# Performance work log

Hardware: AMD Instinct MI355X
Metric: run time of the kernel (lower is better)

## Reference

```python
import jax, jax.numpy as jnp
import numpy as np

N = 50000
E = 800000
IN_DIM = 128
HID = 32
OUT_DIM = 64
HEADS = 4
NEG_SLOPE = 0.2  # DGL GATConv default leaky_relu slope


def setup_inputs() -> dict:
    key = jax.random.key(0)
    ks = jax.random.split(key, 16)
    h = jax.random.normal(ks[0], (N, IN_DIM), dtype=jnp.float32)
    src = jax.random.randint(ks[1], (E,), 0, N, dtype=jnp.int32)
    dst = jax.random.randint(ks[2], (E,), 0, N, dtype=jnp.int32)
    s = 0.05
    # layer 1: in 128 -> heads*32 = 128
    W1 = jax.random.normal(ks[3], (IN_DIM, HEADS * HID), dtype=jnp.float32) * s
    al1 = jax.random.normal(ks[4], (HEADS, HID), dtype=jnp.float32) * s
    ar1 = jax.random.normal(ks[5], (HEADS, HID), dtype=jnp.float32) * s
    # layer 2: in 128 -> heads*32 = 128
    W2 = jax.random.normal(ks[6], (HEADS * HID, HEADS * HID), dtype=jnp.float32) * s
    al2 = jax.random.normal(ks[7], (HEADS, HID), dtype=jnp.float32) * s
    ar2 = jax.random.normal(ks[8], (HEADS, HID), dtype=jnp.float32) * s
    # last layer: in 128 -> heads*64 = 256 (needs residual projection)
    W3 = jax.random.normal(ks[9], (HEADS * HID, HEADS * OUT_DIM), dtype=jnp.float32) * s
    al3 = jax.random.normal(ks[10], (HEADS, OUT_DIM), dtype=jnp.float32) * s
    ar3 = jax.random.normal(ks[11], (HEADS, OUT_DIM), dtype=jnp.float32) * s
    resW3 = jax.random.normal(ks[12], (HEADS * HID, HEADS * OUT_DIM), dtype=jnp.float32) * s
    return {"h": h, "W1": W1, "al1": al1, "ar1": ar1, "W2": W2, "al2": al2,
            "ar2": ar2, "W3": W3, "al3": al3, "ar3": ar3, "resW3": resW3,
            "src": src, "dst": dst}


def gat_layer(h, src, dst, W, al, ar, heads, out_feats, res_W=None, act=None):
    n = h.shape[0]
    feat = (h @ W).reshape(n, heads, out_feats)          # [N,H,D]
    el = jnp.einsum('nhd,hd->nh', feat, al)               # [N,H]
    er = jnp.einsum('nhd,hd->nh', feat, ar)               # [N,H]
    e = jax.nn.leaky_relu(el[src] + er[dst], NEG_SLOPE)   # [E,H]
    m = jax.ops.segment_max(e, dst, num_segments=n)       # per-dst max, [N,H]
    ex = jnp.exp(e - m[dst])
    denom = jax.ops.segment_sum(ex, dst, num_segments=n)  # [N,H]
    alpha = ex / denom[dst]                               # edge softmax, [E,H]
    msg = feat[src] * alpha[:, :, None]                   # [E,H,D]
    rst = jax.ops.segment_sum(msg, dst, num_segments=n)   # [N,H,D]
    res = (h @ res_W) if res_W is not None else h
    rst = rst + res.reshape(n, heads, out_feats)
    if act is not None:
        rst = act(rst)
    return rst


def reference(h, W1, al1, ar1, W2, al2, ar2, W3, al3, ar3, resW3, src, dst):
    n = h.shape[0]
    x = gat_layer(h, src, dst, W1, al1, ar1, HEADS, HID, act=jax.nn.relu)
    x = x.reshape(n, -1)
    # feat_drop=0.3 on layer 2 omitted (eval/deterministic mode)
    x = gat_layer(x, src, dst, W2, al2, ar2, HEADS, HID, act=jax.nn.relu)
    x = x.reshape(n, -1)
    x = gat_layer(x, src, dst, W3, al3, ar3, HEADS, OUT_DIM, res_W=resW3)
    return x.mean(axis=1)  # mean over heads -> [N, OUT_DIM]
```

## Files before the change

### kernel.cpp

```cpp
#include <hip/hip_runtime.h>
#include <hip/hip_bf16.h>
#include <math.h>


#define NEG_SLOPE 0.2f

typedef __attribute__((ext_vector_type(8))) __bf16 bf16x8;
typedef __attribute__((ext_vector_type(4))) float f32x4;

__device__ __forceinline__ float leaky(float x) { return fmaxf(x, NEG_SLOPE * x); }
__device__ __forceinline__ ushort f2bf(float f) {
    unsigned u = __float_as_uint(f);
    return (ushort)((u + 0x7fffu + ((u >> 16) & 1u)) >> 16);
}
__device__ __forceinline__ float bf2f(ushort b) { return __uint_as_float(((unsigned)b) << 16); }
__device__ __forceinline__ float lo16f(unsigned v) { return __uint_as_float(v << 16); }
__device__ __forceinline__ float hi16f(unsigned v) { return __uint_as_float(v & 0xffff0000u); }


__global__ void hist_kernel(const int* __restrict__ dst, int* __restrict__ deg, int E) {
    int i = blockIdx.x * blockDim.x + threadIdx.x;
    if (i < E) atomicAdd(&deg[dst[i]], 1);
}

__global__ void block_scan_kernel(const int* __restrict__ deg, int* __restrict__ loc,
                                  int* __restrict__ bsum, int n) {
    __shared__ int sm[1024];
    const int tid = threadIdx.x;
    const int i = blockIdx.x * 1024 + tid;
    int v = (i < n) ? deg[i] : 0;
    sm[tid] = v;
    __syncthreads();
    for (int off = 1; off < 1024; off <<= 1) {
        int t = (tid >= off) ? sm[tid - off] : 0;
        __syncthreads();
        sm[tid] += t;
        __syncthreads();
    }
    if (i < n) loc[i] = sm[tid] - v;
    if (tid == 1023) bsum[blockIdx.x] = sm[1023];
}

__global__ void apply_scan_kernel(const int* __restrict__ loc, const int* __restrict__ bsum,
                                  int* __restrict__ row_ptr, int* __restrict__ cursor,
                                  int n, int nb) {
    __shared__ int pb[64];
    const int tid = threadIdx.x;
    if (tid < 64) {
        int v = (tid < nb) ? bsum[tid] : 0;
        int orig = v;
        for (int off = 1; off < 64; off <<= 1) {
            int t = __shfl_up(v, off);
            if (tid >= off) v += t;
        }
        pb[tid] = v - orig;
        if (tid == 63 && blockIdx.x == 0) row_ptr[n] = v;
    }
    __syncthreads();
    int i = blockIdx.x * blockDim.x + tid;
    if (i < n) {
        int v = loc[i] + pb[i >> 10];
        row_ptr[i] = v;
        cursor[i]  = v;
    }
}

__global__ void scatter_kernel(const int* __restrict__ src, const int* __restrict__ dst,
                               int* __restrict__ cursor, int* __restrict__ ssrc, int E) {
    int i = blockIdx.x * blockDim.x + threadIdx.x;
    if (i < E) {
        int s = src[i];
        int pos = atomicAdd(&cursor[dst[i]], 1);
        ssrc[pos] = s;
    }
}


__global__ void prep_kernel(const float* __restrict__ h, ushort* __restrict__ xbh,
                            const float* __restrict__ W1, ushort* __restrict__ W1th,
                            const float* __restrict__ W2, ushort* __restrict__ W2th,
                            const float* __restrict__ W3, ushort* __restrict__ W3th,
                            const float* __restrict__ rW3, ushort* __restrict__ rWmh,
                            int* __restrict__ cursor, int nh4, int n) {
    int i = blockIdx.x * blockDim.x + threadIdx.x;
    if (i < nh4) {
        float4 v = ((const float4*)h)[i];
        ushort4 o;
        o.x = f2bf(v.x); o.y = f2bf(v.y); o.z = f2bf(v.z); o.w = f2bf(v.w);
        ((ushort4*)xbh)[i] = o;
        return;
    }
    int j = i - nh4;
    if (j < 16384) {
        int c = j >> 7, k = j & 127;
        int kd = k ^ ((c & 7) << 3);
        W1th[c * 128 + kd] = f2bf(W1[k * 128 + c]);
    } else if (j < 32768) {
        j -= 16384;
        int c = j >> 7, k = j & 127;
        int kd = k ^ ((c & 7) << 3);
        W2th[c * 128 + kd] = f2bf(W2[k * 128 + c]);
    } else if (j < 65536) {
        j -= 32768;
        int c = j >> 7, k = j & 127;
        int kd = k ^ ((c & 7) << 3);
        W3th[c * 128 + kd] = f2bf(W3[k * 256 + c]);
    } else if (j < 73728) {
        j -= 65536;
        int c = j >> 7, k = j & 127;
        const float* row = rW3 + (size_t)k * 256;
        float v = 0.25f * ((row[c] + row[64 + c]) + (row[128 + c] + row[192 + c]));
        int kd = k ^ ((c & 7) << 3);
        rWmh[c * 128 + kd] = f2bf(v);
    } else if (j < 73728 + n) {
        cursor[j - 73728] = 0;
    }
}


__global__ void __launch_bounds__(128)
gemm_kernel(const ushort* __restrict__ Ah, const ushort* __restrict__ Bth,
            const ushort* __restrict__ B2th,
            ushort* __restrict__ Cb, float* __restrict__ C2f,
            const float* __restrict__ alv, const float* __restrict__ arv,
            float* __restrict__ el, float* __restrict__ er,
            int M, int Ncols, int dshift) {
    extern __shared__ ushort Ws[];
    ushort* Ws2 = Ws + 128 * 128;
    const int tid = threadIdx.x;
    const int wv = tid >> 6;
    const int lane = tid & 63;
    const int l15 = lane & 15;
    const int g = lane >> 4;
    const int bm = blockIdx.x * 64 + wv * 32;
    const int bn = blockIdx.y * 128;
    const bool do2 = (B2th != nullptr) && (blockIdx.y == 0);

    {
        const uint4* gh = (const uint4*)(Bth + (size_t)bn * 128);
        uint4* sh = (uint4*)Ws;
#pragma unroll
        for (int it = 0; it < 16; ++it) sh[it * 128 + tid] = gh[it * 128 + tid];
        if (do2) {
            const uint4* g2 = (const uint4*)B2th;
            uint4* s2 = (uint4*)Ws2;
#pragma unroll
            for (int it = 0; it < 8; ++it) s2[it * 128 + tid] = g2[it * 128 + tid];
        }
    }
    __syncthreads();

    const int m0 = bm + l15;
    const int m1 = bm + 16 + l15;
    const int mc0 = (m0 < M) ? m0 : (M - 1);
    const int mc1 = (m1 < M) ? m1 : (M - 1);
    bf16x8 xh[2][4];
#pragma unroll
    for (int kk = 0; kk < 4; ++kk) {
        xh[0][kk] = *(const bf16x8*)(Ah + (size_t)mc0 * 128 + kk * 32 + g * 8);
        xh[1][kk] = *(const bf16x8*)(Ah + (size_t)mc1 * 128 + kk * 32 + g * 8);
    }

    f32x4 acc[2][8] = {};
    f32x4 acc2[2][4] = {};
    const int swz = (l15 & 7) << 4;
#pragma unroll
    for (int n = 0; n < 8; ++n) {
        const int colb = (n * 16 + l15) * 256;
#pragma unroll
        for (int kk = 0; kk < 4; ++kk) {
            const int boff = colb + ((kk * 64 + g * 16) ^ swz);
            bf16x8 wh = *(const bf16x8*)((const char*)Ws + boff);
            acc[0][n] = __builtin_amdgcn_mfma_f32_16x16x32_bf16(wh, xh[0][kk], acc[0][n], 0, 0, 0);
            acc[1][n] = __builtin_amdgcn_mfma_f32_16x16x32_bf16(wh, xh[1][kk], acc[1][n], 0, 0, 0);
        }
    }
    if (do2) {
#pragma unroll
        for (int n = 0; n < 4; ++n) {
            const int colb = (n * 16 + l15) * 256;
#pragma unroll
            for (int kk = 0; kk < 4; ++kk) {
                const int boff = colb + ((kk * 64 + g * 16) ^ swz);
                bf16x8 w2 = *(const bf16x8*)((const char*)Ws2 + boff);
                acc2[0][n] = __builtin_amdgcn_mfma_f32_16x16x32_bf16(w2, xh[0][kk], acc2[0][n], 0, 0, 0);
                acc2[1][n] = __builtin_amdgcn_mfma_f32_16x16x32_bf16(w2, xh[1][kk], acc2[1][n], 0, 0, 0);
            }
        }
    }

#pragma unroll
    for (int mf = 0; mf < 2; ++mf) {
        const int m = (mf == 0) ? m0 : m1;
        const bool valid = (m < M);
        if (valid) {
            size_t ro = (size_t)m * Ncols;
#pragma unroll
            for (int n = 0; n < 8; ++n) {
                int col = bn + n * 16 + g * 4;
                ushort4 o;
                o.x = f2bf(acc[mf][n][0]); o.y = f2bf(acc[mf][n][1]);
                o.z = f2bf(acc[mf][n][2]); o.w = f2bf(acc[mf][n][3]);
                *(ushort4*)&Cb[ro + col] = o;
            }
            if (do2) {
#pragma unroll
                for (int n = 0; n < 4; ++n) {
                    *(float4*)&C2f[(size_t)m * 64 + n * 16 + g * 4] =
                        make_float4(acc2[mf][n][0], acc2[mf][n][1],
                                    acc2[mf][n][2], acc2[mf][n][3]);
                }
            }
        }
        if (alv) {
            float e0 = 0.f, e1 = 0.f, e2 = 0.f, e3 = 0.f;
            float r0 = 0.f, r1 = 0.f, r2 = 0.f, r3 = 0.f;
            const bool four = (dshift == 5);
#pragma unroll
            for (int n = 0; n < 8; ++n) {
                float se = 0.f, sr = 0.f;
#pragma unroll
                for (int rr = 0; rr < 4; ++rr) {
                    int col = bn + n * 16 + g * 4 + rr;
                    float c = acc[mf][n][rr];
                    se += c * alv[col];
                    sr += c * arv[col];
                }
                if (four) {
                    if (n < 2)      { e0 += se; r0 += sr; }
                    else if (n < 4) { e1 += se; r1 += sr; }
                    else if (n < 6) { e2 += se; r2 += sr; }
                    else            { e3 += se; r3 += sr; }
                } else {
                    if (n < 4)      { e0 += se; r0 += sr; }
                    else            { e1 += se; r1 += sr; }
                }
            }
            e0 += __shfl_xor(e0, 16); e0 += __shfl_xor(e0, 32);
            e1 += __shfl_xor(e1, 16); e1 += __shfl_xor(e1, 32);
            r0 += __shfl_xor(r0, 16); r0 += __shfl_xor(r0, 32);
            r1 += __shfl_xor(r1, 16); r1 += __shfl_xor(r1, 32);
            if (four) {
                e2 += __shfl_xor(e2, 16); e2 += __shfl_xor(e2, 32);
                e3 += __shfl_xor(e3, 16); e3 += __shfl_xor(e3, 32);
                r2 += __shfl_xor(r2, 16); r2 += __shfl_xor(r2, 32);
                r3 += __shfl_xor(r3, 16); r3 += __shfl_xor(r3, 32);
            }
            if (valid && g == 0) {
                if (four) {
                    el[m * 4 + 0] = e0; el[m * 4 + 1] = e1;
                    el[m * 4 + 2] = e2; el[m * 4 + 3] = e3;
                    er[m * 4 + 0] = r0; er[m * 4 + 1] = r1;
                    er[m * 4 + 2] = r2; er[m * 4 + 3] = r3;
                } else {
                    int h0 = bn >> 6;
                    el[m * 4 + h0] = e0; el[m * 4 + h0 + 1] = e1;
                    er[m * 4 + h0] = r0; er[m * 4 + h0 + 1] = r1;
                }
            }
        }
    }
}


__global__ void __launch_bounds__(256)
aggregate12_kernel(const ushort* __restrict__ featb, const float* __restrict__ el,
                   const float* __restrict__ er, const int* __restrict__ row_ptr,
                   const int* __restrict__ ssrc, const float* __restrict__ resf,
                   const ushort* __restrict__ rxh, const ushort* __restrict__ rxl,
                   ushort* __restrict__ xbh, ushort* __restrict__ xbl, int n) {
    const int wid = threadIdx.x >> 6;
    const int lane = threadIdx.x & 63;
    const int node = blockIdx.x * 4 + wid;
    if (node >= n) return;
    const int beg = row_ptr[node];
    const int end = row_ptr[node + 1];
    const int hh = lane >> 4;
    const float erh = er[node * 4 + hh];

    float ssum = 0.f, a0 = 0.f, a1 = 0.f;
    int p = beg;
    for (; p + 8 <= end; p += 8) {
        int s[8];
        float e[8];
        unsigned v[8];
#pragma unroll
        for (int j = 0; j < 8; ++j) s[j] = __builtin_amdgcn_readfirstlane(ssrc[p + j]);
#pragma unroll
        for (int j = 0; j < 8; ++j) v[j] = *(const unsigned*)&featb[(size_t)s[j] * 128 + lane * 2];
#pragma unroll
        for (int j = 0; j < 8; ++j) e[j] = el[s[j] * 4 + hh];
#pragma unroll
        for (int j = 0; j < 8; ++j) {
            float w0 = __expf(leaky(e[j] + erh));
            ssum += w0;
            a0 += w0 * lo16f(v[j]);
            a1 += w0 * hi16f(v[j]);
        }
    }
    for (; p < end; ++p) {
        int s = __builtin_amdgcn_readfirstlane(ssrc[p]);
        float w0 = __expf(leaky(el[s * 4 + hh] + erh));
        unsigned v = *(const unsigned*)&featb[(size_t)s * 128 + lane * 2];
        ssum += w0;
        a0 += w0 * lo16f(v);
        a1 += w0 * hi16f(v);
    }
    float inv = (end > beg) ? 1.f / ssum : 0.f;
    size_t o = (size_t)node * 128 + lane * 2;
    float rb0, rb1;
    if (resf) {
        float2 f = *(const float2*)&resf[o];
        rb0 = f.x; rb1 = f.y;
    } else {
        unsigned rh = *(const unsigned*)&rxh[o];
        unsigned rl = *(const unsigned*)&rxl[o];
        rb0 = lo16f(rh) + lo16f(rl);
        rb1 = hi16f(rh) + hi16f(rl);
    }
    float r0 = fmaxf(a0 * inv + rb0, 0.f);
    float r1 = fmaxf(a1 * inv + rb1, 0.f);
    ushort h0 = f2bf(r0), h1 = f2bf(r1);
    ushort l0 = f2bf(r0 - bf2f(h0)), l1 = f2bf(r1 - bf2f(h1));
    *(unsigned*)&xbh[o] = (unsigned)h0 | ((unsigned)h1 << 16);
    *(unsigned*)&xbl[o] = (unsigned)l0 | ((unsigned)l1 << 16);
}


__global__ void __launch_bounds__(256)
aggregate3_kernel(const ushort* __restrict__ featb, const float* __restrict__ el,
                  const float* __restrict__ er, const int* __restrict__ row_ptr,
                  const int* __restrict__ ssrc, const float* __restrict__ resmean,
                  float* __restrict__ out, int n) {
    const int wid = threadIdx.x >> 6;
    const int lane = threadIdx.x & 63;
    const int node = blockIdx.x * 4 + wid;
    if (node >= n) return;
    const int beg = row_ptr[node];
    const int end = row_ptr[node + 1];
    const int hh = lane >> 4;
    const int dd = (lane & 15) * 4;
    const int off = hh * 64 + dd;
    const float erh = er[node * 4 + hh];

    float c0 = 0.f, c1 = 0.f, c2 = 0.f, c3 = 0.f, ssum = 0.f;
    int p = beg;
    for (; p + 8 <= end; p += 8) {
        int s[8];
        float e[8];
        uint2 v[8];
#pragma unroll
        for (int j = 0; j < 8; ++j) s[j] = __builtin_amdgcn_readfirstlane(ssrc[p + j]);
#pragma unroll
        for (int j = 0; j < 8; ++j) v[j] = *(const uint2*)&featb[(size_t)s[j] * 256 + off];
#pragma unroll
        for (int j = 0; j < 8; ++j) e[j] = el[s[j] * 4 + hh];
#pragma unroll
        for (int j = 0; j < 8; ++j) {
            float w0 = __expf(leaky(e[j] + erh));
            ssum += w0;
            c0 += w0 * lo16f(v[j].x);
            c1 += w0 * hi16f(v[j].x);
            c2 += w0 * lo16f(v[j].y);
            c3 += w0 * hi16f(v[j].y);
        }
    }
    for (; p < end; ++p) {
        int s = __builtin_amdgcn_readfirstlane(ssrc[p]);
        float w0 = __expf(leaky(el[s * 4 + hh] + erh));
        uint2 v = *(const uint2*)&featb[(size_t)s * 256 + off];
        ssum += w0;
        c0 += w0 * lo16f(v.x);
        c1 += w0 * hi16f(v.x);
        c2 += w0 * lo16f(v.y);
        c3 += w0 * hi16f(v.y);
    }
    float inv = (end > beg) ? 1.f / ssum : 0.f;
    float r0 = c0 * inv, r1 = c1 * inv, r2 = c2 * inv, r3 = c3 * inv;
    r0 += __shfl_xor(r0, 16); r0 += __shfl_xor(r0, 32);
    r1 += __shfl_xor(r1, 16); r1 += __shfl_xor(r1, 32);
    r2 += __shfl_xor(r2, 16); r2 += __shfl_xor(r2, 32);
    r3 += __shfl_xor(r3, 16); r3 += __shfl_xor(r3, 32);
    if (hh == 0) {
        float4 rm = *(const float4*)&resmean[(size_t)node * 64 + dd];
        *(float4*)&out[(size_t)node * 64 + dd] =
            make_float4(0.25f * r0 + rm.x, 0.25f * r1 + rm.y,
                        0.25f * r2 + rm.z, 0.25f * r3 + rm.w);
    }
}


extern "C" void kernel_launch(void* const* d_in, const int* in_sizes, int n_in,
                              void* d_out, int out_size, void* d_ws, size_t ws_size,
                              hipStream_t stream) {
    const float* h   = (const float*)d_in[0];
    const float* W1  = (const float*)d_in[1];
    const float* al1 = (const float*)d_in[2];
    const float* ar1 = (const float*)d_in[3];
    const float* W2  = (const float*)d_in[4];
    const float* al2 = (const float*)d_in[5];
    const float* ar2 = (const float*)d_in[6];
    const float* W3  = (const float*)d_in[7];
    const float* al3 = (const float*)d_in[8];
    const float* ar3 = (const float*)d_in[9];
    const float* rW3 = (const float*)d_in[10];
    const int* src   = (const int*)d_in[11];
    const int* dstv  = (const int*)d_in[12];
    const int N = in_sizes[0] / 128;
    const int E = in_sizes[11];
    float* out = (float*)d_out;

    char* p = (char*)d_ws;
    auto alloc = [&](size_t bytes) -> char* {
        char* q = p;
        p += (bytes + 255) & ~(size_t)255;
        return q;
    };
    int*    row_ptr = (int*)alloc((size_t)(N + 1) * 4);
    int*    cursor  = (int*)alloc((size_t)N * 4);
    int*    loc     = (int*)alloc((size_t)N * 4);
    int*    bsum    = (int*)alloc(64 * 4);
    int*    ssrc    = (int*)alloc((size_t)E * 4);
    float*  el      = (float*)alloc((size_t)N * 16);
    float*  er      = (float*)alloc((size_t)N * 16);
    ushort* featb   = (ushort*)alloc((size_t)N * 256 * 2);
    ushort* xbh     = (ushort*)alloc((size_t)N * 128 * 2);
    ushort* xbl     = (ushort*)alloc((size_t)N * 128 * 2);
    ushort* W1th = (ushort*)alloc(128 * 128 * 2);
    ushort* W2th = (ushort*)alloc(128 * 128 * 2);
    ushort* W3th = (ushort*)alloc(256 * 128 * 2);
    ushort* rWmh = (ushort*)alloc(64 * 128 * 2);
    float*  resmean = (float*)alloc((size_t)N * 64 * 4);

    const int nh4 = N * 32;
    const int prep_total = nh4 + 73728 + N;
    prep_kernel<<<(prep_total + 255) / 256, 256, 0, stream>>>(
        h, xbh, W1, W1th, W2, W2th, W3, W3th, rW3, rWmh, cursor, nh4, N);

    hist_kernel<<<(E + 255) / 256, 256, 0, stream>>>(dstv, cursor, E);
    int nb = (N + 1023) / 1024;
    block_scan_kernel<<<nb, 1024, 0, stream>>>(cursor, loc, bsum, N);
    apply_scan_kernel<<<(N + 255) / 256, 256, 0, stream>>>(loc, bsum, row_ptr, cursor, N, nb);
    scatter_kernel<<<(E + 255) / 256, 256, 0, stream>>>(src, dstv, cursor, ssrc, E);

    const int gx = (N + 63) / 64;
    dim3 g1(gx, 1);
    dim3 g3(gx, 2);
    int agg_grid = (N + 3) / 4;
    const size_t lds1 = 128 * 128 * sizeof(ushort);
    const size_t lds3 = (128 * 128 + 64 * 128) * sizeof(ushort);

    gemm_kernel<<<g1, 128, lds1, stream>>>(xbh, W1th, nullptr, featb, nullptr,
                                           al1, ar1, el, er, N, 128, 5);
    aggregate12_kernel<<<agg_grid, 256, 0, stream>>>(featb, el, er, row_ptr, ssrc,
                                                     h, nullptr, nullptr, xbh, xbl, N);

    gemm_kernel<<<g1, 128, lds1, stream>>>(xbh, W2th, nullptr, featb, nullptr,
                                           al2, ar2, el, er, N, 128, 5);
    aggregate12_kernel<<<agg_grid, 256, 0, stream>>>(featb, el, er, row_ptr, ssrc,
                                                     nullptr, xbh, xbl, xbh, xbl, N);

    gemm_kernel<<<g3, 128, lds3, stream>>>(xbh, W3th, rWmh, featb, resmean,
                                           al3, ar3, el, er, N, 256, 6);
    aggregate3_kernel<<<agg_grid, 256, 0, stream>>>(featb, el, er, row_ptr, ssrc, resmean, out, N);
}
```

Baseline: 395.3 us.

## Split each wavefront into two half-waves processing alternate edges in aggregation

Both aggregation kernels now have the two 32-lane halves of a wavefront gather different edges at once. Each lane loads wider vectors (8 or 16 bytes) covering more features, and the halves combine their partial sums with a cross-half shuffle at the end. The goal is more independent gathers in flight per wave and fewer, wider loads, so the latency-bound edge loop runs shorter. In exchange, edge indices are no longer wave-uniform scalar loads, and extra shuffle reductions plus a masked tail are added.

```diff
diff --git a/kernel.cpp b/kernel.cpp
--- a/kernel.cpp
+++ b/kernel.cpp
@@ -275,55 +275,78 @@
     if (node >= n) return;
     const int beg = row_ptr[node];
     const int end = row_ptr[node + 1];
-    const int hh = lane >> 4;
+    const int half = lane >> 5;
+    const int l32 = lane & 31;
+    const int hh = l32 >> 3;
     const float erh = er[node * 4 + hh];
 
-    float ssum = 0.f, a0 = 0.f, a1 = 0.f;
+    float ssum = 0.f, a0 = 0.f, a1 = 0.f, a2 = 0.f, a3 = 0.f;
     int p = beg;
     for (; p + 8 <= end; p += 8) {
-        int s[8];
-        float e[8];
-        unsigned v[8];
-#pragma unroll
-        for (int j = 0; j < 8; ++j) s[j] = __builtin_amdgcn_readfirstlane(ssrc[p + j]);
-#pragma unroll
-        for (int j = 0; j < 8; ++j) v[j] = *(const unsigned*)&featb[(size_t)s[j] * 128 + lane * 2];
-#pragma unroll
-        for (int j = 0; j < 8; ++j) e[j] = el[s[j] * 4 + hh];
-#pragma unroll
-        for (int j = 0; j < 8; ++j) {
-            float w0 = __expf(leaky(e[j] + erh));
-            ssum += w0;
-            a0 += w0 * lo16f(v[j]);
-            a1 += w0 * hi16f(v[j]);
-        }
-    }
-    for (; p < end; ++p) {
-        int s = __builtin_amdgcn_readfirstlane(ssrc[p]);
-        float w0 = __expf(leaky(el[s * 4 + hh] + erh));
-        unsigned v = *(const unsigned*)&featb[(size_t)s * 128 + lane * 2];
-        ssum += w0;
-        a0 += w0 * lo16f(v);
-        a1 += w0 * hi16f(v);
-    }
+        int s[4]; uint2 v[4]; float e[4];
+#pragma unroll
+        for (int j = 0; j < 4; ++j) s[j] = ssrc[p + 2 * j + half];
+#pragma unroll
+        for (int j = 0; j < 4; ++j) v[j] = *(const uint2*)&featb[(size_t)s[j] * 128 + l32 * 4];
+#pragma unroll
+        for (int j = 0; j < 4; ++j) e[j] = el[s[j] * 4 + hh];
+#pragma unroll
+        for (int j = 0; j < 4; ++j) {
+            float w = __expf(leaky(e[j] + erh));
+            ssum += w;
+            a0 += w * lo16f(v[j].x);
+            a1 += w * hi16f(v[j].x);
+            a2 += w * lo16f(v[j].y);
+            a3 += w * hi16f(v[j].y);
+        }
+    }
+    for (; p < end; p += 2) {
+        int pe = p + half;
+        bool ok = pe < end;
+        int s = ssrc[ok ? pe : beg];
+        uint2 v = *(const uint2*)&featb[(size_t)s * 128 + l32 * 4];
+        float w = ok ? __expf(leaky(el[s * 4 + hh] + erh)) : 0.f;
+        ssum += w;
+        a0 += w * lo16f(v.x);
+        a1 += w * hi16f(v.x);
+        a2 += w * lo16f(v.y);
+        a3 += w * hi16f(v.y);
+    }
+    ssum += __shfl_xor(ssum, 32);
+    a0 += __shfl_xor(a0, 32);
+    a1 += __shfl_xor(a1, 32);
+    a2 += __shfl_xor(a2, 32);
+    a3 += __shfl_xor(a3, 32);
     float inv = (end > beg) ? 1.f / ssum : 0.f;
-    size_t o = (size_t)node * 128 + lane * 2;
-    float rb0, rb1;
-    if (resf) {
-        float2 f = *(const float2*)&resf[o];
-        rb0 = f.x; rb1 = f.y;
-    } else {
-        unsigned rh = *(const unsigned*)&rxh[o];
-        unsigned rl = *(const unsigned*)&rxl[o];
-        rb0 = lo16f(rh) + lo16f(rl);
-        rb1 = hi16f(rh) + hi16f(rl);
-    }
-    float r0 = fmaxf(a0 * inv + rb0, 0.f);
-    float r1 = fmaxf(a1 * inv + rb1, 0.f);
-    ushort h0 = f2bf(r0), h1 = f2bf(r1);
-    ushort l0 = f2bf(r0 - bf2f(h0)), l1 = f2bf(r1 - bf2f(h1));
-    *(unsigned*)&xbh[o] = (unsigned)h0 | ((unsigned)h1 << 16);
-    *(unsigned*)&xbl[o] = (unsigned)l0 | ((unsigned)l1 << 16);
+    if (half == 0) {
+        size_t o = (size_t)node * 128 + l32 * 4;
+        float rb0, rb1, rb2, rb3;
+        if (resf) {
+            float4 f = *(const float4*)&resf[o];
+            rb0 = f.x; rb1 = f.y; rb2 = f.z; rb3 = f.w;
+        } else {
+            uint2 rh = *(const uint2*)&rxh[o];
+            uint2 rl = *(const uint2*)&rxl[o];
+            rb0 = lo16f(rh.x) + lo16f(rl.x);
+            rb1 = hi16f(rh.x) + hi16f(rl.x);
+            rb2 = lo16f(rh.y) + lo16f(rl.y);
+            rb3 = hi16f(rh.y) + hi16f(rl.y);
+        }
+        float r0 = fmaxf(a0 * inv + rb0, 0.f);
+        float r1 = fmaxf(a1 * inv + rb1, 0.f);
+        float r2 = fmaxf(a2 * inv + rb2, 0.f);
+        float r3 = fmaxf(a3 * inv + rb3, 0.f);
+        ushort h0 = f2bf(r0), h1 = f2bf(r1), h2 = f2bf(r2), h3 = f2bf(r3);
+        ushort l0 = f2bf(r0 - bf2f(h0)), l1 = f2bf(r1 - bf2f(h1));
+        ushort l2 = f2bf(r2 - bf2f(h2)), l3 = f2bf(r3 - bf2f(h3));
+        uint2 oh, ol;
+        oh.x = (unsigned)h0 | ((unsigned)h1 << 16);
+        oh.y = (unsigned)h2 | ((unsigned)h3 << 16);
+        ol.x = (unsigned)l0 | ((unsigned)l1 << 16);
+        ol.y = (unsigned)l2 | ((unsigned)l3 << 16);
+        *(uint2*)&xbh[o] = oh;
+        *(uint2*)&xbl[o] = ol;
+    }
 }
 
 
@@ -338,54 +361,64 @@
     if (node >= n) return;
     const int beg = row_ptr[node];
     const int end = row_ptr[node + 1];
-    const int hh = lane >> 4;
-    const int dd = (lane & 15) * 4;
-    const int off = hh * 64 + dd;
+    const int half = lane >> 5;
+    const int l32 = lane & 31;
+    const int hh = l32 >> 3;
     const float erh = er[node * 4 + hh];
 
-    float c0 = 0.f, c1 = 0.f, c2 = 0.f, c3 = 0.f, ssum = 0.f;
+    float c[8] = {};
+    float ssum = 0.f;
     int p = beg;
     for (; p + 8 <= end; p += 8) {
-        int s[8];
-        float e[8];
-        uint2 v[8];
-#pragma unroll
-        for (int j = 0; j < 8; ++j) s[j] = __builtin_amdgcn_readfirstlane(ssrc[p + j]);
-#pragma unroll
-        for (int j = 0; j < 8; ++j) v[j] = *(const uint2*)&featb[(size_t)s[j] * 256 + off];
-#pragma unroll
-        for (int j = 0; j < 8; ++j) e[j] = el[s[j] * 4 + hh];
-#pragma unroll
-        for (int j = 0; j < 8; ++j) {
-            float w0 = __expf(leaky(e[j] + erh));
-            ssum += w0;
-            c0 += w0 * lo16f(v[j].x);
-            c1 += w0 * hi16f(v[j].x);
-            c2 += w0 * lo16f(v[j].y);
-            c3 += w0 * hi16f(v[j].y);
-        }
-    }
-    for (; p < end; ++p) {
-        int s = __builtin_amdgcn_readfirstlane(ssrc[p]);
-        float w0 = __expf(leaky(el[s * 4 + hh] + erh));
-        uint2 v = *(const uint2*)&featb[(size_t)s * 256 + off];
-        ssum += w0;
-        c0 += w0 * lo16f(v.x);
-        c1 += w0 * hi16f(v.x);
-        c2 += w0 * lo16f(v.y);
-        c3 += w0 * hi16f(v.y);
-    }
+        int s[4]; uint4 v[4]; float e[4];
+#pragma unroll
+        for (int j = 0; j < 4; ++j) s[j] = ssrc[p + 2 * j + half];
+#pragma unroll
+        for (int j = 0; j < 4; ++j) v[j] = *(const uint4*)&featb[(size_t)s[j] * 256 + l32 * 8];
+#pragma unroll
+        for (int j = 0; j < 4; ++j) e[j] = el[s[j] * 4 + hh];
+#pragma unroll
+        for (int j = 0; j < 4; ++j) {
+            float w = __expf(leaky(e[j] + erh));
+            ssum += w;
+            c[0] += w * lo16f(v[j].x); c[1] += w * hi16f(v[j].x);
+            c[2] += w * lo16f(v[j].y); c[3] += w * hi16f(v[j].y);
+            c[4] += w * lo16f(v[j].z); c[5] += w * hi16f(v[j].z);
+            c[6] += w * lo16f(v[j].w); c[7] += w * hi16f(v[j].w);
+        }
+    }
+    for (; p < end; p += 2) {
+        int pe = p + half;
+        bool ok = pe < end;
+        int s = ssrc[ok ? pe : beg];
+        uint4 v = *(const uint4*)&featb[(size_t)s * 256 + l32 * 8];
+        float w = ok ? __expf(leaky(el[s * 4 + hh] + erh)) : 0.f;
+        ssum += w;
+        c[0] += w * lo16f(v.x); c[1] += w * hi16f(v.x);
+        c[2] += w * lo16f(v.y); c[3] += w * hi16f(v.y);
+        c[4] += w * lo16f(v.z); c[5] += w * hi16f(v.z);
+        c[6] += w * lo16f(v.w); c[7] += w * hi16f(v.w);
+    }
+    ssum += __shfl_xor(ssum, 32);
+#pragma unroll
+    for (int i = 0; i < 8; ++i) c[i] += __shfl_xor(c[i], 32);
     float inv = (end > beg) ? 1.f / ssum : 0.f;
-    float r0 = c0 * inv, r1 = c1 * inv, r2 = c2 * inv, r3 = c3 * inv;
-    r0 += __shfl_xor(r0, 16); r0 += __shfl_xor(r0, 32);
-    r1 += __shfl_xor(r1, 16); r1 += __shfl_xor(r1, 32);
-    r2 += __shfl_xor(r2, 16); r2 += __shfl_xor(r2, 32);
-    r3 += __shfl_xor(r3, 16); r3 += __shfl_xor(r3, 32);
-    if (hh == 0) {
-        float4 rm = *(const float4*)&resmean[(size_t)node * 64 + dd];
-        *(float4*)&out[(size_t)node * 64 + dd] =
-            make_float4(0.25f * r0 + rm.x, 0.25f * r1 + rm.y,
-                        0.25f * r2 + rm.z, 0.25f * r3 + rm.w);
+#pragma unroll
+    for (int i = 0; i < 8; ++i) c[i] *= inv;
+#pragma unroll
+    for (int i = 0; i < 8; ++i) c[i] += __shfl_xor(c[i], 8);
+#pragma unroll
+    for (int i = 0; i < 8; ++i) c[i] += __shfl_xor(c[i], 16);
+    if (lane < 8) {
+        const int d0 = lane * 8;
+        float4 rm0 = *(const float4*)&resmean[(size_t)node * 64 + d0];
+        float4 rm1 = *(const float4*)&resmean[(size_t)node * 64 + d0 + 4];
+        *(float4*)&out[(size_t)node * 64 + d0] =
+            make_float4(0.25f * c[0] + rm0.x, 0.25f * c[1] + rm0.y,
+                        0.25f * c[2] + rm0.z, 0.25f * c[3] + rm0.w);
+        *(float4*)&out[(size_t)node * 64 + d0 + 4] =
+            make_float4(0.25f * c[4] + rm1.x, 0.25f * c[5] + rm1.y,
+                        0.25f * c[6] + rm1.z, 0.25f * c[7] + rm1.w);
     }
 }
 
```

Result: no change. 390.1 us (-1.3%).
